# Kernel tuning notes

Measured on AMD Instinct MI355X. Metric: run time of the kernel, lower is better.

## Reference

```python
import jax, jax.numpy as jnp
import numpy as np

B, T, H = 4, 4096, 2048
G_EPS = 0.5
LN_EPS = 1e-5
INIT_STD = 0.02


def setup_inputs() -> dict:
    key = jax.random.key(0)
    ks = jax.random.split(key, 4)
    return {
        "hidden_states": jax.random.normal(ks[0], (B, T, H), jnp.float32),
        "W_z": jax.random.normal(ks[1], (H, H), jnp.float32) * INIT_STD,
        "b_z": jnp.zeros((H,), jnp.float32),
        "W_h": jax.random.normal(ks[2], (H, H), jnp.float32) * INIT_STD,
        "b_h": jnp.zeros((H,), jnp.float32),
        "ln_w": jnp.ones((H,), jnp.float32),
        "ln_b": jnp.zeros((H,), jnp.float32),
        "h0": jax.random.normal(ks[3], (H,), jnp.float32) * INIT_STD,
    }


def _g_log(x):
    # torch.where(x >= 0, log(relu(x) + g_eps), -softplus(-x))
    return jnp.where(x >= 0, jnp.log(jax.nn.relu(x) + G_EPS), -jax.nn.softplus(-x))


def reference(hidden_states, W_z, b_z, W_h, b_h, ln_w, ln_b, h0):
    Bc, Tc, Hc = hidden_states.shape
    k = hidden_states @ W_z.T + b_z                      # [B,T,H]
    log_z = -jax.nn.softplus(-k)                         # log sigmoid(k)
    log_coeffs = -jax.nn.softplus(k)                     # log(1 - sigmoid(k))
    log_tilde_h = _g_log(hidden_states @ W_h.T + b_h)    # [B,T,H]
    log_h0 = jnp.broadcast_to(_g_log(h0), (Bc, 1, Hc))
    log_values = jnp.concatenate([log_h0, log_z + log_tilde_h], axis=1)  # [B,T+1,H]
    # NOTE: faithful to source: cumsum over the LAST (hidden) dim, then pad one
    # zero row at the front of the time dim (F.pad(..., (0,0,1,0))).
    a_star = jnp.pad(jnp.cumsum(log_coeffs, axis=-1), ((0, 0), (1, 0), (0, 0)))  # [B,T+1,H]
    log_h = a_star + jax.lax.cumlogsumexp(log_values - a_star, axis=1)
    # global mean / unbiased std normalization, as in source
    log_h = (log_h - log_h.mean()) / jnp.std(log_h, ddof=1)
    h = jnp.exp(log_h)[:, 1:, :]                         # drop the h0 step
    # residual + LayerNorm (dropout is identity in eval)
    x = h + hidden_states
    mu = x.mean(axis=-1, keepdims=True)
    var = x.var(axis=-1, keepdims=True)
    return (x - mu) * jax.lax.rsqrt(var + LN_EPS) * ln_w + ln_b
```

## Files before the change

### kernel.cpp

```cpp
#include <hip/hip_runtime.h>
#include <stdint.h>

constexpr int NB = 4;
constexpr int NT = 4096;
constexpr int NH = 2048;
constexpr int MROWS = NB * NT;
constexpr int TP1 = NT + 1;
constexpr int CH2 = 16;
constexpr int NCH2 = (TP1 + CH2 - 1) / CH2;

typedef unsigned short u16;
typedef __bf16 bf16x8 __attribute__((ext_vector_type(8)));
typedef float f32x4 __attribute__((ext_vector_type(4)));
typedef unsigned short u16x8 __attribute__((ext_vector_type(8)));
typedef u16x8 __attribute__((may_alias)) u16x8_a;
typedef float4 __attribute__((may_alias)) float4_a;

__device__ __forceinline__ u16 f2bf(float f) {
  unsigned int u = __float_as_uint(f);
  return (u16)((u + 0x7fffu + ((u >> 16) & 1u)) >> 16);
}
__device__ __forceinline__ float bf2f(u16 v) {
  return __uint_as_float(((unsigned int)v) << 16);
}
__device__ __forceinline__ float spf_(float x) {
  return fmaxf(x, 0.f) + __logf(1.f + __expf(-fabsf(x)));
}
__device__ __forceinline__ float glogf_(float x) {
  return (x >= 0.f) ? __logf(x + 0.5f) : -spf_(-x);
}
__device__ __forceinline__ void gld16(const void* g, void* l) {
  __builtin_amdgcn_global_load_lds((const __attribute__((address_space(1))) void*)g,
                                   (__attribute__((address_space(3))) void*)l, 16, 0, 0);
}
__device__ __forceinline__ void ld8(const float* p, float* r) {
  float4 a = *(const float4_a*)p, b = *(const float4_a*)(p + 4);
  r[0] = a.x; r[1] = a.y; r[2] = a.z; r[3] = a.w;
  r[4] = b.x; r[5] = b.y; r[6] = b.z; r[7] = b.w;
}
__device__ __forceinline__ void st8(float* p, const float* r) {
  *(float4_a*)p       = make_float4(r[0], r[1], r[2], r[3]);
  *(float4_a*)(p + 4) = make_float4(r[4], r[5], r[6], r[7]);
}

__global__ __launch_bounds__(256) void cvt_all(
    const float* __restrict__ hs, const float* __restrict__ Wz,
    const float* __restrict__ Wh, u16* __restrict__ hsb,
    u16* __restrict__ wzb, u16* __restrict__ whb) {
  const int s0 = MROWS * NH / 8;
  const int s1 = s0 + NH * NH / 8;
  const int s2 = s1 + NH * NH / 8;
  int i = blockIdx.x * 256 + threadIdx.x;
  if (i >= s2) return;
  const float* in; u16* out; int j;
  if (i < s0)      { in = hs; out = hsb; j = i; }
  else if (i < s1) { in = Wz; out = wzb; j = i - s0; }
  else             { in = Wh; out = whb; j = i - s1; }
  const float4* p = (const float4*)in;
  float4 a = p[2 * (size_t)j], b = p[2 * (size_t)j + 1];
  u16x8 o;
  o[0] = f2bf(a.x); o[1] = f2bf(a.y); o[2] = f2bf(a.z); o[3] = f2bf(a.w);
  o[4] = f2bf(b.x); o[5] = f2bf(b.y); o[6] = f2bf(b.z); o[7] = f2bf(b.w);
  *(u16x8*)(out + (size_t)j * 8) = o;
}

__global__ __launch_bounds__(256, 3) void gemm_bt(
    const u16* __restrict__ A,
    const u16* __restrict__ Bz, const u16* __restrict__ Bh,
    const float* __restrict__ bz, const float* __restrict__ bh,
    u16* __restrict__ KU) {
  const u16* Bm  = blockIdx.y ? Bh : Bz;
  const float* bias = blockIdx.y ? bh : bz;
  u16* Cw = KU + (blockIdx.y ? 2048 : 0);

  const int bid = blockIdx.x;
  const int wg = (bid & 7) * 256 + (bid >> 3);
  const int bx = wg & 15;
  const int by = wg >> 4;
  const int row0 = by << 7, col0 = bx << 7;

  __shared__ u16 ldsA[128 * 64];
  __shared__ u16 ldsB[128 * 64];

  const int tid = threadIdx.x;
  const int lane = tid & 63;
  const int wv = tid >> 6;
  const int wr = (wv >> 1) << 6;
  const int wc = (wv & 1) << 6;

  const int srow = lane >> 3;
  const int sslot = ((lane & 7) ^ srow) << 3;
  const int xsw = (lane & 7) << 3;
  const int q8 = (lane >> 4) << 3;
  const int f15 = lane & 15;

  f32x4 acc[4][4] = {};

  for (int k0 = 0; k0 < NH; k0 += 64) {
    if (k0) __syncthreads();
#pragma unroll
    for (int i = 0; i < 4; ++i) {
      const int r = i * 32 + wv * 8 + srow;
      const size_t gcol = (size_t)(k0 + sslot);
      gld16(A  + (size_t)(row0 + r) * NH + gcol, &ldsA[(size_t)(i * 256 + wv * 64) * 8]);
      gld16(Bm + (size_t)(col0 + r) * NH + gcol, &ldsB[(size_t)(i * 256 + wv * 64) * 8]);
    }
    __syncthreads();
#pragma unroll
    for (int ks = 0; ks < 2; ++ks) {
      const int cphys = ((ks << 5) | q8) ^ xsw;
      bf16x8 af[4], bfr[4];
#pragma unroll
      for (int m = 0; m < 4; ++m)
        af[m] = *(const bf16x8*)&ldsA[(wr + m * 16 + f15) * 64 + cphys];
#pragma unroll
      for (int n = 0; n < 4; ++n)
        bfr[n] = *(const bf16x8*)&ldsB[(wc + n * 16 + f15) * 64 + cphys];
#pragma unroll
      for (int m = 0; m < 4; ++m)
#pragma unroll
        for (int n = 0; n < 4; ++n)
          acc[m][n] = __builtin_amdgcn_mfma_f32_16x16x32_bf16(af[m], bfr[n], acc[m][n], 0, 0, 0);
    }
  }

  const int fr = lane & 15, fq = lane >> 4;
#pragma unroll
  for (int n = 0; n < 4; ++n) {
    const int col = col0 + wc + n * 16 + fr;
    const float bv = bias[col];
#pragma unroll
    for (int m = 0; m < 4; ++m) {
#pragma unroll
      for (int v = 0; v < 4; ++v) {
        const int row = row0 + wr + m * 16 + fq * 4 + v;
        Cw[(size_t)row * 4096 + col] = f2bf(acc[m][n][v] + bv);
      }
    }
  }
}

__global__ __launch_bounds__(256) void scan_fused(
    char* __restrict__ KU, float* __restrict__ UD,
    float* __restrict__ Z0, float* __restrict__ cm, float* __restrict__ cs,
    const float* __restrict__ h0) {
  const int ch = blockIdx.x;
  const int b = blockIdx.y;
  const int tid = threadIdx.x;
  const int lane = tid & 63, wvx = tid >> 6;
  const int t0 = ch * CH2;
  const int t1 = (t0 + CH2 < TP1) ? (t0 + CH2) : TP1;

  float m8[8], s8[8];
#pragma unroll
  for (int e = 0; e < 8; ++e) { m8[e] = -INFINITY; s8[e] = 0.f; }

  __shared__ float wsum[2][4];

  float lc[8], lv[8];
  {
    const int tf = (t0 < 1) ? 1 : t0;
    if (tf < t1) {
      const size_t rb = ((size_t)b * NT + (tf - 1)) * 8192;
      u16x8 kv = *(const u16x8_a*)(KU + rb + tid * 16);
      u16x8 uv = *(const u16x8_a*)(KU + rb + 4096 + tid * 16);
#pragma unroll
      for (int e = 0; e < 8; ++e) {
        const float k = bf2f(kv[e]);
        const float L = __logf(1.f + __expf(-fabsf(k)));
        lc[e] = -fmaxf(k, 0.f) - L;
        lv[e] = fminf(k, 0.f) - L + glogf_(bf2f(uv[e]));
      }
    }
  }

  for (int tt = t0; tt < t1; ++tt) {
    if (tt == 0) {
#pragma unroll
      for (int e = 0; e < 8; ++e) {
        const float x = glogf_(h0[tid * 8 + e]);
        m8[e] = x; s8[e] = 1.f;
        Z0[(size_t)b * NH + tid * 8 + e] = x;
      }
      continue;
    }
    float nlc[8], nlv[8];
    const bool pf = (tt + 1 < t1);
    if (pf) {
      const size_t rb = ((size_t)b * NT + tt) * 8192;
      u16x8 kv = *(const u16x8_a*)(KU + rb + tid * 16);
      u16x8 uv = *(const u16x8_a*)(KU + rb + 4096 + tid * 16);
#pragma unroll
      for (int e = 0; e < 8; ++e) {
        const float k = bf2f(kv[e]);
        const float L = __logf(1.f + __expf(-fabsf(k)));
        nlc[e] = -fmaxf(k, 0.f) - L;
        nlv[e] = fminf(k, 0.f) - L + glogf_(bf2f(uv[e]));
      }
    }
    float cum[8], run = 0.f;
#pragma unroll
    for (int e = 0; e < 8; ++e) { run += lc[e]; cum[e] = run; }
    float v = run;
#pragma unroll
    for (int d = 1; d < 64; d <<= 1) {
      float o = __shfl_up(v, d, 64);
      if (lane >= d) v += o;
    }
    const int par = tt & 1;
    if (lane == 63) wsum[par][wvx] = v;
    __syncthreads();
    float base = v - run;
#pragma unroll
    for (int w = 0; w < 4; ++w)
      if (w < wvx) base += wsum[par][w];

    const size_t row = (size_t)b * NT + (tt - 1);
    float as8[8], L8[8];
#pragma unroll
    for (int e = 0; e < 8; ++e) {
      const float as = base + cum[e];
      as8[e] = as;
      const float x = lv[e] - as;
      const float nm = fmaxf(m8[e], x);
      s8[e] = s8[e] * __expf(m8[e] - nm) + __expf(x - nm);
      m8[e] = nm;
      L8[e] = nm + __logf(s8[e]);
    }
    st8((float*)(KU + row * 8192) + tid * 8, as8);
    st8(UD + row * NH + tid * 8, L8);
    if (pf) {
#pragma unroll
      for (int e = 0; e < 8; ++e) { lc[e] = nlc[e]; lv[e] = nlv[e]; }
    }
  }
  const size_t co = ((size_t)ch * NB + b) * NH + tid * 8;
  st8(cm + co, m8);
  st8(cs + co, s8);
}

__global__ __launch_bounds__(256) void carryscan(float* __restrict__ cm,
                                                 float* __restrict__ cs) {
  const int c = blockIdx.x * 256 + threadIdx.x;
  const int b = c >> 11;
  const int hh = c & (NH - 1);
  float Cm = -INFINITY, Cs = 0.f;
  size_t o = ((size_t)0 * NB + b) * NH + hh;
  float m2 = cm[o], s2 = cs[o];
  for (int ch = 0; ch < NCH2; ++ch) {
    float nm2, ns2;
    if (ch + 1 < NCH2) {
      const size_t on = ((size_t)(ch + 1) * NB + b) * NH + hh;
      nm2 = cm[on]; ns2 = cs[on];
    }
    cm[o] = Cm; cs[o] = Cs;
    const float M = fmaxf(Cm, m2);
    Cs = Cs * __expf(Cm - M) + s2 * __expf(m2 - M);
    Cm = M;
    o = ((size_t)(ch + 1) * NB + b) * NH + hh;
    m2 = nm2; s2 = ns2;
  }
}

__global__ __launch_bounds__(256) void combine_stats(
    float* __restrict__ LL, const float* __restrict__ Z0,
    const float* __restrict__ cm, const float* __restrict__ cs,
    const float* __restrict__ AS, double* __restrict__ sums) {
  const int ch = blockIdx.x;
  const int b = blockIdx.y;
  const int tid = threadIdx.x;
  const int h8 = tid * 8;
  const size_t co = ((size_t)ch * NB + b) * NH + h8;
  float Cm8[8], Cs8[8];
  ld8(cm + co, Cm8);
  ld8(cs + co, Cs8);
  const int t0 = ch * CH2;
  const int t1 = (t0 + CH2 < TP1) ? (t0 + CH2) : TP1;

  double s1 = 0.0, s2 = 0.0;
  float L8[8], as8[8];
  {
    const int tf = (t0 < 1) ? 1 : t0;
    if (tf < t1) {
      const size_t off = ((size_t)b * NT + (tf - 1)) * NH + h8;
      ld8(LL + off, L8);
      ld8(AS + off, as8);
    }
  }
  for (int tt = t0; tt < t1; ++tt) {
    if (tt == 0) {
      float z8[8];
      ld8(Z0 + (size_t)b * NH + h8, z8);
#pragma unroll
      for (int e = 0; e < 8; ++e) {
        const float M = fmaxf(z8[e], Cm8[e]);
        const float lh = M + __logf(__expf(z8[e] - M) + Cs8[e] * __expf(Cm8[e] - M));
        s1 += (double)lh;
        s2 += (double)lh * (double)lh;
      }
      continue;
    }
    float nL8[8], nas8[8];
    const bool pf = (tt + 1 < t1);
    if (pf) {
      const size_t noff = ((size_t)b * NT + tt) * NH + h8;
      ld8(LL + noff, nL8);
      ld8(AS + noff, nas8);
    }
    const size_t off = ((size_t)b * NT + (tt - 1)) * NH + h8;
    float o8[8];
#pragma unroll
    for (int e = 0; e < 8; ++e) {
      const float M = fmaxf(L8[e], Cm8[e]);
      const float lse = M + __logf(__expf(L8[e] - M) + Cs8[e] * __expf(Cm8[e] - M));
      const float lh = as8[e] + lse;
      o8[e] = lh;
      s1 += (double)lh;
      s2 += (double)lh * (double)lh;
    }
    st8(LL + off, o8);
    if (pf) {
#pragma unroll
      for (int e = 0; e < 8; ++e) { L8[e] = nL8[e]; as8[e] = nas8[e]; }
    }
  }
  double v1 = s1, v2 = s2;
#pragma unroll
  for (int d = 32; d; d >>= 1) {
    v1 += __shfl_down(v1, d, 64);
    v2 += __shfl_down(v2, d, 64);
  }
  __shared__ double dr1[4], dr2[4];
  const int lane = threadIdx.x & 63, wvx = threadIdx.x >> 6;
  if (lane == 0) { dr1[wvx] = v1; dr2[wvx] = v2; }
  __syncthreads();
  if (threadIdx.x == 0) {
    atomicAdd(&sums[0], dr1[0] + dr1[1] + dr1[2] + dr1[3]);
    atomicAdd(&sums[1], dr2[0] + dr2[1] + dr2[2] + dr2[3]);
  }
}

__global__ void finalize_stats(const double* __restrict__ sums,
                               float* __restrict__ stats) {
  const double S = sums[0], S2 = sums[1];
  const double N = (double)NB * (double)TP1 * (double)NH;
  const double mu = S / N;
  const double var = (S2 - S * S / N) / (N - 1.0);
  stats[0] = (float)mu;
  stats[1] = (float)(1.0 / sqrt(var));
}

__global__ __launch_bounds__(256) void final_ln(float* __restrict__ LL,
                                                const float* __restrict__ hs,
                                                const float* __restrict__ lnw,
                                                const float* __restrict__ lnb,
                                                const float* __restrict__ stats) {
  const int tid = threadIdx.x;
  const size_t off = (size_t)blockIdx.x * NH + tid * 8;
  const float mu_g = stats[0], isd = stats[1];

  float lh[8], av[8];
  ld8(LL + off, lh);
  ld8(hs + off, av);
  float x[8];
  float s = 0.f, q = 0.f;
#pragma unroll
  for (int e = 0; e < 8; ++e) {
    x[e] = __expf((lh[e] - mu_g) * isd) + av[e];
    s += x[e];
    q += x[e] * x[e];
  }
#pragma unroll
  for (int d = 32; d; d >>= 1) {
    s += __shfl_down(s, d, 64);
    q += __shfl_down(q, d, 64);
  }
  __shared__ float r1[4], r2[4];
  const int lane = tid & 63, wvx = tid >> 6;
  if (lane == 0) { r1[wvx] = s; r2[wvx] = q; }
  __syncthreads();
  const float st = r1[0] + r1[1] + r1[2] + r1[3];
  const float qt = r2[0] + r2[1] + r2[2] + r2[3];
  const float mean = st * (1.0f / NH);
  const float var = qt * (1.0f / NH) - mean * mean;
  const float rstd = rsqrtf(var + 1e-5f);

  float wv8[8], bv8[8];
  ld8(lnw + tid * 8, wv8);
  ld8(lnb + tid * 8, bv8);
  float o[8];
#pragma unroll
  for (int e = 0; e < 8; ++e)
    o[e] = (x[e] - mean) * rstd * wv8[e] + bv8[e];
  st8(LL + off, o);
}

extern "C" void kernel_launch(void* const* d_in, const int* in_sizes, int n_in,
                              void* d_out, int out_size, void* d_ws, size_t ws_size,
                              hipStream_t stream) {
  (void)in_sizes; (void)n_in; (void)out_size; (void)ws_size;
  const float* hs  = (const float*)d_in[0];
  const float* Wz  = (const float*)d_in[1];
  const float* bz  = (const float*)d_in[2];
  const float* Wh  = (const float*)d_in[3];
  const float* bh  = (const float*)d_in[4];
  const float* lnw = (const float*)d_in[5];
  const float* lnb = (const float*)d_in[6];
  const float* h0  = (const float*)d_in[7];
  float* out = (float*)d_out;

  char* w = (char*)d_ws;
  u16* hsb   = (u16*)w;  w += (size_t)MROWS * NH * 2;
  u16* wzb   = (u16*)w;  w += (size_t)NH * NH * 2;
  u16* whb   = (u16*)w;  w += (size_t)NH * NH * 2;
  char* KU   = w;        w += (size_t)MROWS * 8192;
  float* Z0   = (float*)w; w += (size_t)NB * NH * 4;
  double* sums = (double*)w; w += 16;
  float* stats = (float*)w;  w += 16;
  float* cm_ = (float*)hsb;
  float* cs_ = cm_ + (size_t)NCH2 * NB * NH;

  hipMemsetAsync(sums, 0, 16, stream);

  {
    const int tot8 = MROWS * NH / 8 + 2 * (NH * NH / 8);
    cvt_all<<<dim3((tot8 + 255) / 256), 256, 0, stream>>>(hs, Wz, Wh, hsb, wzb, whb);
  }

  gemm_bt<<<dim3((MROWS / 128) * (NH / 128), 2), 256, 0, stream>>>(
      hsb, wzb, whb, bz, bh, (u16*)KU);

  scan_fused<<<dim3(NCH2, NB), 256, 0, stream>>>(KU, out, Z0, cm_, cs_, h0);

  carryscan<<<dim3(NB * NH / 256), 256, 0, stream>>>(cm_, cs_);

  combine_stats<<<dim3(NCH2, NB), 256, 0, stream>>>(out, Z0, cm_, cs_, (float*)KU, sums);
  finalize_stats<<<1, 1, 0, stream>>>(sums, stats);

  final_ln<<<dim3(MROWS), 256, 0, stream>>>(out, hs, lnw, lnb, stats);
}
```

Baseline: 636.0 us.

## Rewrite GEMM as 256x128 tile, 8-wave, triple-buffered ping-pong pipeline

Replaces the 128x128 single-buffered GEMM with a 256x128 tile run by 8 waves. K tiles are prefetched two steps ahead into a triple-buffered LDS ring with partial vmcnt waits. Each step is split into two MFMA phases separated by barriers, with s_setprio raised during the MFMA phases so global loads overlap compute. This targets load latency stalls and the sync-per-tile overhead, but uses much more LDS (144KB per block), which limits occupancy, and relies on fragile hand-set barrier and waitcnt ordering.

After: 662.9 us. +4.2%, slower.

```diff
diff --git a/kernel.cpp b/kernel.cpp
--- a/kernel.cpp
+++ b/kernel.cpp
@@ -8,6 +8,7 @@
 constexpr int TP1 = NT + 1;
 constexpr int CH2 = 16;
 constexpr int NCH2 = (TP1 + CH2 - 1) / CH2;
+constexpr int NKT = NH / 64;
 
 typedef unsigned short u16;
 typedef __bf16 bf16x8 __attribute__((ext_vector_type(8)));
@@ -64,7 +65,7 @@
   *(u16x8*)(out + (size_t)j * 8) = o;
 }
 
-__global__ __launch_bounds__(256, 3) void gemm_bt(
+__global__ __launch_bounds__(512, 2) void gemm_8ph(
     const u16* __restrict__ A,
     const u16* __restrict__ Bz, const u16* __restrict__ Bh,
     const float* __restrict__ bz, const float* __restrict__ bh,
@@ -74,66 +75,112 @@
   u16* Cw = KU + (blockIdx.y ? 2048 : 0);
 
   const int bid = blockIdx.x;
-  const int wg = (bid & 7) * 256 + (bid >> 3);
+  const int wg = (bid & 7) * 128 + (bid >> 3);
   const int bx = wg & 15;
   const int by = wg >> 4;
-  const int row0 = by << 7, col0 = bx << 7;
-
-  __shared__ u16 ldsA[128 * 64];
-  __shared__ u16 ldsB[128 * 64];
+  const int row0 = by << 8, col0 = bx << 7;
+
+  __shared__ u16 ldsA[3][256 * 64];
+  __shared__ u16 ldsB[3][128 * 64];
 
   const int tid = threadIdx.x;
   const int lane = tid & 63;
   const int wv = tid >> 6;
-  const int wr = (wv >> 1) << 6;
-  const int wc = (wv & 1) << 6;
-
-  const int srow = lane >> 3;
-  const int sslot = ((lane & 7) ^ srow) << 3;
+  const int wrow = (wv >> 1) << 6;
+  const int wcol = (wv & 1) << 6;
+
+  const int srow = tid >> 3;
+  const int sslot = ((tid & 7) ^ (srow & 7)) << 3;
   const int xsw = (lane & 7) << 3;
   const int q8 = (lane >> 4) << 3;
   const int f15 = lane & 15;
 
+#define STAGE_A(sb, tg, r)                                                     \
+  gld16(A + (size_t)(row0 + ((r) << 6) + srow) * NH + (((tg) << 6) + sslot),   \
+        &ldsA[sb][(((r) << 9) + (wv << 6)) * 8])
+#define STAGE_B(sb, tg, r)                                                     \
+  gld16(Bm + (size_t)(col0 + ((r) << 6) + srow) * NH + (((tg) << 6) + sslot),  \
+        &ldsB[sb][(((r) << 9) + (wv << 6)) * 8])
+
   f32x4 acc[4][4] = {};
 
-  for (int k0 = 0; k0 < NH; k0 += 64) {
-    if (k0) __syncthreads();
-#pragma unroll
-    for (int i = 0; i < 4; ++i) {
-      const int r = i * 32 + wv * 8 + srow;
-      const size_t gcol = (size_t)(k0 + sslot);
-      gld16(A  + (size_t)(row0 + r) * NH + gcol, &ldsA[(size_t)(i * 256 + wv * 64) * 8]);
-      gld16(Bm + (size_t)(col0 + r) * NH + gcol, &ldsB[(size_t)(i * 256 + wv * 64) * 8]);
-    }
-    __syncthreads();
-#pragma unroll
-    for (int ks = 0; ks < 2; ++ks) {
-      const int cphys = ((ks << 5) | q8) ^ xsw;
-      bf16x8 af[4], bfr[4];
-#pragma unroll
-      for (int m = 0; m < 4; ++m)
-        af[m] = *(const bf16x8*)&ldsA[(wr + m * 16 + f15) * 64 + cphys];
+  STAGE_A(0, 0, 0); STAGE_A(0, 0, 1); STAGE_A(0, 0, 2); STAGE_A(0, 0, 3);
+  STAGE_B(0, 0, 0); STAGE_B(0, 0, 1);
+  STAGE_A(1, 1, 0); STAGE_A(1, 1, 1); STAGE_A(1, 1, 2); STAGE_A(1, 1, 3);
+  STAGE_B(1, 1, 0); STAGE_B(1, 1, 1);
+  asm volatile("s_waitcnt vmcnt(6)");
+  __builtin_amdgcn_sched_barrier(0);
+  __builtin_amdgcn_s_barrier();
+
+  for (int g = 0; g < NKT; ++g) {
+    const int buf = g % 3;
+    const int sb = (g + 2) % 3;
+    const bool st = (g + 2) < NKT;
+    const u16* la = ldsA[buf];
+    const u16* lb = ldsB[buf];
+
+    bf16x8 bfr[4][2], af0[2][2];
+#pragma unroll
+    for (int n = 0; n < 4; ++n)
+#pragma unroll
+      for (int kk = 0; kk < 2; ++kk)
+        bfr[n][kk] = *(const bf16x8*)&lb[(wcol + n * 16 + f15) * 64 + (((kk << 5) | q8) ^ xsw)];
+#pragma unroll
+    for (int m = 0; m < 2; ++m)
+#pragma unroll
+      for (int kk = 0; kk < 2; ++kk)
+        af0[m][kk] = *(const bf16x8*)&la[(wrow + m * 16 + f15) * 64 + (((kk << 5) | q8) ^ xsw)];
+    if (st) { STAGE_A(sb, g + 2, 0); STAGE_A(sb, g + 2, 1); STAGE_A(sb, g + 2, 2); }
+    __builtin_amdgcn_s_barrier();
+    __builtin_amdgcn_s_setprio(1);
+#pragma unroll
+    for (int m = 0; m < 2; ++m)
 #pragma unroll
       for (int n = 0; n < 4; ++n)
-        bfr[n] = *(const bf16x8*)&ldsB[(wc + n * 16 + f15) * 64 + cphys];
-#pragma unroll
-      for (int m = 0; m < 4; ++m)
-#pragma unroll
-        for (int n = 0; n < 4; ++n)
-          acc[m][n] = __builtin_amdgcn_mfma_f32_16x16x32_bf16(af[m], bfr[n], acc[m][n], 0, 0, 0);
-    }
-  }
+#pragma unroll
+        for (int kk = 0; kk < 2; ++kk)
+          acc[m][n] = __builtin_amdgcn_mfma_f32_16x16x32_bf16(af0[m][kk], bfr[n][kk], acc[m][n], 0, 0, 0);
+    __builtin_amdgcn_s_setprio(0);
+    __builtin_amdgcn_s_barrier();
+
+    bf16x8 af1[2][2];
+#pragma unroll
+    for (int m = 0; m < 2; ++m)
+#pragma unroll
+      for (int kk = 0; kk < 2; ++kk)
+        af1[m][kk] = *(const bf16x8*)&la[(wrow + (m + 2) * 16 + f15) * 64 + (((kk << 5) | q8) ^ xsw)];
+    if (st) { STAGE_A(sb, g + 2, 3); STAGE_B(sb, g + 2, 0); STAGE_B(sb, g + 2, 1); }
+    __builtin_amdgcn_s_barrier();
+    __builtin_amdgcn_s_setprio(1);
+#pragma unroll
+    for (int m = 0; m < 2; ++m)
+#pragma unroll
+      for (int n = 0; n < 4; ++n)
+#pragma unroll
+        for (int kk = 0; kk < 2; ++kk)
+          acc[m + 2][n] = __builtin_amdgcn_mfma_f32_16x16x32_bf16(af1[m][kk], bfr[n][kk], acc[m + 2][n], 0, 0, 0);
+    __builtin_amdgcn_s_setprio(0);
+    if (g < NKT - 3) {
+      asm volatile("s_waitcnt vmcnt(6)");
+    } else {
+      asm volatile("s_waitcnt vmcnt(0)");
+    }
+    __builtin_amdgcn_sched_barrier(0);
+    __builtin_amdgcn_s_barrier();
+  }
+#undef STAGE_A
+#undef STAGE_B
 
   const int fr = lane & 15, fq = lane >> 4;
 #pragma unroll
   for (int n = 0; n < 4; ++n) {
-    const int col = col0 + wc + n * 16 + fr;
+    const int col = col0 + wcol + n * 16 + fr;
     const float bv = bias[col];
 #pragma unroll
     for (int m = 0; m < 4; ++m) {
 #pragma unroll
       for (int v = 0; v < 4; ++v) {
-        const int row = row0 + wr + m * 16 + fq * 4 + v;
+        const int row = row0 + wrow + m * 16 + fq * 4 + v;
         Cw[(size_t)row * 4096 + col] = f2bf(acc[m][n][v] + bv);
       }
     }
@@ -427,7 +474,7 @@
     cvt_all<<<dim3((tot8 + 255) / 256), 256, 0, stream>>>(hs, Wz, Wh, hsb, wzb, whb);
   }
 
-  gemm_bt<<<dim3((MROWS / 128) * (NH / 128), 2), 256, 0, stream>>>(
+  gemm_8ph<<<dim3((MROWS / 256) * (NH / 128), 2), 512, 0, stream>>>(
       hsb, wzb, whb, bz, bh, (u16*)KU);
 
   scan_fused<<<dim3(NCH2, NB), 256, 0, stream>>>(KU, out, Z0, cm_, cs_, h0);
```

## Recompute scan in second pass instead of materializing intermediate prefix and LSE arrays

Applied to the files above, without the earlier changes.

The chunked log-space scan is split into a carry-only first pass that stores just the per-chunk max and sum. A second pass reseeds from the scanned carries, recomputes the pointwise logs and prefix sums, and emits final log_h together with the global statistics. This removes the write and re-read of the fp32 a_star and partial-LSE arrays and the Z0 buffer, roughly halving global traffic for the scan stages. The cost is that the transcendental pointwise work and the block-level prefix scan now run twice.

New measurement: 618.3 us. -2.8%, faster.

```diff
diff --git a/kernel.cpp b/kernel.cpp
--- a/kernel.cpp
+++ b/kernel.cpp
@@ -140,9 +140,22 @@
   }
 }
 
-__global__ __launch_bounds__(256) void scan_fused(
-    char* __restrict__ KU, float* __restrict__ UD,
-    float* __restrict__ Z0, float* __restrict__ cm, float* __restrict__ cs,
+__device__ __forceinline__ void row_pointwise(const char* KU, size_t row,
+                                              int tid, float* lc, float* lv) {
+  const size_t rb = row * 8192;
+  u16x8 kv = *(const u16x8_a*)(KU + rb + tid * 16);
+  u16x8 uv = *(const u16x8_a*)(KU + rb + 4096 + tid * 16);
+#pragma unroll
+  for (int e = 0; e < 8; ++e) {
+    const float k = bf2f(kv[e]);
+    const float L = __logf(1.f + __expf(-fabsf(k)));
+    lc[e] = -fmaxf(k, 0.f) - L;
+    lv[e] = fminf(k, 0.f) - L + glogf_(bf2f(uv[e]));
+  }
+}
+
+__global__ __launch_bounds__(256) void carry_pass(
+    const char* __restrict__ KU, float* __restrict__ cm, float* __restrict__ cs,
     const float* __restrict__ h0) {
   const int ch = blockIdx.x;
   const int b = blockIdx.y;
@@ -160,18 +173,7 @@
   float lc[8], lv[8];
   {
     const int tf = (t0 < 1) ? 1 : t0;
-    if (tf < t1) {
-      const size_t rb = ((size_t)b * NT + (tf - 1)) * 8192;
-      u16x8 kv = *(const u16x8_a*)(KU + rb + tid * 16);
-      u16x8 uv = *(const u16x8_a*)(KU + rb + 4096 + tid * 16);
-#pragma unroll
-      for (int e = 0; e < 8; ++e) {
-        const float k = bf2f(kv[e]);
-        const float L = __logf(1.f + __expf(-fabsf(k)));
-        lc[e] = -fmaxf(k, 0.f) - L;
-        lv[e] = fminf(k, 0.f) - L + glogf_(bf2f(uv[e]));
-      }
-    }
+    if (tf < t1) row_pointwise(KU, (size_t)b * NT + (tf - 1), tid, lc, lv);
   }
 
   for (int tt = t0; tt < t1; ++tt) {
@@ -180,24 +182,13 @@
       for (int e = 0; e < 8; ++e) {
         const float x = glogf_(h0[tid * 8 + e]);
         m8[e] = x; s8[e] = 1.f;
-        Z0[(size_t)b * NH + tid * 8 + e] = x;
       }
       continue;
     }
     float nlc[8], nlv[8];
     const bool pf = (tt + 1 < t1);
-    if (pf) {
-      const size_t rb = ((size_t)b * NT + tt) * 8192;
-      u16x8 kv = *(const u16x8_a*)(KU + rb + tid * 16);
-      u16x8 uv = *(const u16x8_a*)(KU + rb + 4096 + tid * 16);
-#pragma unroll
-      for (int e = 0; e < 8; ++e) {
-        const float k = bf2f(kv[e]);
-        const float L = __logf(1.f + __expf(-fabsf(k)));
-        nlc[e] = -fmaxf(k, 0.f) - L;
-        nlv[e] = fminf(k, 0.f) - L + glogf_(bf2f(uv[e]));
-      }
-    }
+    if (pf) row_pointwise(KU, (size_t)b * NT + tt, tid, nlc, nlv);
+
     float cum[8], run = 0.f;
 #pragma unroll
     for (int e = 0; e < 8; ++e) { run += lc[e]; cum[e] = run; }
@@ -215,20 +206,13 @@
     for (int w = 0; w < 4; ++w)
       if (w < wvx) base += wsum[par][w];
 
-    const size_t row = (size_t)b * NT + (tt - 1);
-    float as8[8], L8[8];
 #pragma unroll
     for (int e = 0; e < 8; ++e) {
-      const float as = base + cum[e];
-      as8[e] = as;
-      const float x = lv[e] - as;
+      const float x = lv[e] - (base + cum[e]);
       const float nm = fmaxf(m8[e], x);
       s8[e] = s8[e] * __expf(m8[e] - nm) + __expf(x - nm);
       m8[e] = nm;
-      L8[e] = nm + __logf(s8[e]);
-    }
-    st8((float*)(KU + row * 8192) + tid * 8, as8);
-    st8(UD + row * NH + tid * 8, L8);
+    }
     if (pf) {
 #pragma unroll
       for (int e = 0; e < 8; ++e) { lc[e] = nlc[e]; lv[e] = nlv[e]; }
@@ -262,66 +246,82 @@
   }
 }
 
-__global__ __launch_bounds__(256) void combine_stats(
-    float* __restrict__ LL, const float* __restrict__ Z0,
+__global__ __launch_bounds__(256) void scan_final(
+    const char* __restrict__ KU, float* __restrict__ LH,
     const float* __restrict__ cm, const float* __restrict__ cs,
-    const float* __restrict__ AS, double* __restrict__ sums) {
+    const float* __restrict__ h0, double* __restrict__ sums) {
   const int ch = blockIdx.x;
   const int b = blockIdx.y;
   const int tid = threadIdx.x;
-  const int h8 = tid * 8;
-  const size_t co = ((size_t)ch * NB + b) * NH + h8;
-  float Cm8[8], Cs8[8];
-  ld8(cm + co, Cm8);
-  ld8(cs + co, Cs8);
+  const int lane = tid & 63, wvx = tid >> 6;
   const int t0 = ch * CH2;
   const int t1 = (t0 + CH2 < TP1) ? (t0 + CH2) : TP1;
 
+  float m8[8], s8[8];
+  {
+    const size_t co = ((size_t)ch * NB + b) * NH + tid * 8;
+    ld8(cm + co, m8);
+    ld8(cs + co, s8);
+  }
+
+  __shared__ float wsum[2][4];
   double s1 = 0.0, s2 = 0.0;
-  float L8[8], as8[8];
+
+  float lc[8], lv[8];
   {
     const int tf = (t0 < 1) ? 1 : t0;
-    if (tf < t1) {
-      const size_t off = ((size_t)b * NT + (tf - 1)) * NH + h8;
-      ld8(LL + off, L8);
-      ld8(AS + off, as8);
-    }
-  }
+    if (tf < t1) row_pointwise(KU, (size_t)b * NT + (tf - 1), tid, lc, lv);
+  }
+
   for (int tt = t0; tt < t1; ++tt) {
     if (tt == 0) {
-      float z8[8];
-      ld8(Z0 + (size_t)b * NH + h8, z8);
 #pragma unroll
       for (int e = 0; e < 8; ++e) {
-        const float M = fmaxf(z8[e], Cm8[e]);
-        const float lh = M + __logf(__expf(z8[e] - M) + Cs8[e] * __expf(Cm8[e] - M));
-        s1 += (double)lh;
-        s2 += (double)lh * (double)lh;
+        const float x = glogf_(h0[tid * 8 + e]);
+        m8[e] = x; s8[e] = 1.f;
+        s1 += (double)x;
+        s2 += (double)x * (double)x;
       }
       continue;
     }
-    float nL8[8], nas8[8];
+    float nlc[8], nlv[8];
     const bool pf = (tt + 1 < t1);
-    if (pf) {
-      const size_t noff = ((size_t)b * NT + tt) * NH + h8;
-      ld8(LL + noff, nL8);
-      ld8(AS + noff, nas8);
-    }
-    const size_t off = ((size_t)b * NT + (tt - 1)) * NH + h8;
-    float o8[8];
+    if (pf) row_pointwise(KU, (size_t)b * NT + tt, tid, nlc, nlv);
+
+    float cum[8], run = 0.f;
+#pragma unroll
+    for (int e = 0; e < 8; ++e) { run += lc[e]; cum[e] = run; }
+    float v = run;
+#pragma unroll
+    for (int d = 1; d < 64; d <<= 1) {
+      float o = __shfl_up(v, d, 64);
+      if (lane >= d) v += o;
+    }
+    const int par = tt & 1;
+    if (lane == 63) wsum[par][wvx] = v;
+    __syncthreads();
+    float base = v - run;
+#pragma unroll
+    for (int w = 0; w < 4; ++w)
+      if (w < wvx) base += wsum[par][w];
+
+    float lh8[8];
 #pragma unroll
     for (int e = 0; e < 8; ++e) {
-      const float M = fmaxf(L8[e], Cm8[e]);
-      const float lse = M + __logf(__expf(L8[e] - M) + Cs8[e] * __expf(Cm8[e] - M));
-      const float lh = as8[e] + lse;
-      o8[e] = lh;
+      const float as = base + cum[e];
+      const float x = lv[e] - as;
+      const float nm = fmaxf(m8[e], x);
+      s8[e] = s8[e] * __expf(m8[e] - nm) + __expf(x - nm);
+      m8[e] = nm;
+      const float lh = as + nm + __logf(s8[e]);
+      lh8[e] = lh;
       s1 += (double)lh;
       s2 += (double)lh * (double)lh;
     }
-    st8(LL + off, o8);
+    st8(LH + ((size_t)b * NT + (tt - 1)) * NH + tid * 8, lh8);
     if (pf) {
 #pragma unroll
-      for (int e = 0; e < 8; ++e) { L8[e] = nL8[e]; as8[e] = nas8[e]; }
+      for (int e = 0; e < 8; ++e) { lc[e] = nlc[e]; lv[e] = nlv[e]; }
     }
   }
   double v1 = s1, v2 = s2;
@@ -331,10 +331,9 @@
     v2 += __shfl_down(v2, d, 64);
   }
   __shared__ double dr1[4], dr2[4];
-  const int lane = threadIdx.x & 63, wvx = threadIdx.x >> 6;
   if (lane == 0) { dr1[wvx] = v1; dr2[wvx] = v2; }
   __syncthreads();
-  if (threadIdx.x == 0) {
+  if (tid == 0) {
     atomicAdd(&sums[0], dr1[0] + dr1[1] + dr1[2] + dr1[3]);
     atomicAdd(&sums[1], dr2[0] + dr2[1] + dr2[2] + dr2[3]);
   }
@@ -414,7 +413,6 @@
   u16* wzb   = (u16*)w;  w += (size_t)NH * NH * 2;
   u16* whb   = (u16*)w;  w += (size_t)NH * NH * 2;
   char* KU   = w;        w += (size_t)MROWS * 8192;
-  float* Z0   = (float*)w; w += (size_t)NB * NH * 4;
   double* sums = (double*)w; w += 16;
   float* stats = (float*)w;  w += 16;
   float* cm_ = (float*)hsb;
@@ -430,11 +428,11 @@
   gemm_bt<<<dim3((MROWS / 128) * (NH / 128), 2), 256, 0, stream>>>(
       hsb, wzb, whb, bz, bh, (u16*)KU);
 
-  scan_fused<<<dim3(NCH2, NB), 256, 0, stream>>>(KU, out, Z0, cm_, cs_, h0);
+  carry_pass<<<dim3(NCH2, NB), 256, 0, stream>>>(KU, cm_, cs_, h0);
 
   carryscan<<<dim3(NB * NH / 256), 256, 0, stream>>>(cm_, cs_);
 
-  combine_stats<<<dim3(NCH2, NB), 256, 0, stream>>>(out, Z0, cm_, cs_, (float*)KU, sums);
+  scan_final<<<dim3(NCH2, NB), 256, 0, stream>>>(KU, out, cm_, cs_, h0, sums);
   finalize_stats<<<1, 1, 0, stream>>>(sums, stats);
 
   final_ln<<<dim3(MROWS), 256, 0, stream>>>(out, hs, lnw, lnb, stats);
```
